# Kernel tuning notes

Measured on AMD Instinct MI355X. Metric: run time of the kernel, lower is better.

The kernel has to match this reference:

```python
import jax, jax.numpy as jnp
import numpy as np

B, S, D = 2, 2048, 2048
H = 16
KV_RANK = 512
NOPE, ROPE = 128, 64
QK_HD = NOPE + ROPE  # 192
V_HD = 128
SCALE = QK_HD ** -0.5
EPS = 1.1920929e-07  # torch RMSNorm default eps = finfo(fp32).eps
NEG = -1e9


def rmsnorm(x, w):
    return x * jax.lax.rsqrt(jnp.mean(x * x, axis=-1, keepdims=True) + EPS) * w


def apply_rope(x, freqs):
    # x: (b, s, h, r) interleaved pairs; freqs: (s, r//2) angles
    sh = x.shape
    xr = x.reshape(*sh[:-1], -1, 2)
    a, b = xr[..., 0], xr[..., 1]
    cos = jnp.cos(freqs)[None, :, None, :]
    sin = jnp.sin(freqs)[None, :, None, :]
    return jnp.stack([a * cos - b * sin, a * sin + b * cos], axis=-1).reshape(sh)


def setup_inputs() -> dict:
    key = jax.random.key(0)
    ks = jax.random.split(key, 8)
    inv = lambda k, shape, fan_in: jax.random.uniform(k, shape, jnp.float32, -1.0, 1.0) / np.sqrt(fan_in)
    x = jax.random.normal(ks[0], (B, S, D), jnp.float32)
    freqs = jax.random.uniform(ks[1], (S, ROPE // 2), jnp.float32) * np.float32(np.pi)
    mask = jnp.where(jnp.triu(jnp.ones((S, S), bool), k=1), jnp.float32(NEG), jnp.float32(0.0))
    wq_w = inv(ks[2], (H * QK_HD, D), D)
    wq_b = jnp.zeros((H * QK_HD,), jnp.float32)
    wkv_a_w = inv(ks[3], (KV_RANK + ROPE, D), D)
    wkv_a_b = jnp.zeros((KV_RANK + ROPE,), jnp.float32)
    kv_norm_w = jnp.ones((KV_RANK,), jnp.float32)
    wkv_b_w = inv(ks[4], (H * (NOPE + V_HD), KV_RANK), KV_RANK)
    wo_w = inv(ks[5], (D, H * V_HD), H * V_HD)
    wo_b = jnp.zeros((D,), jnp.float32)
    return dict(x=x, freqs=freqs, mask=mask, wq_w=wq_w, wq_b=wq_b,
                wkv_a_w=wkv_a_w, wkv_a_b=wkv_a_b, kv_norm_w=kv_norm_w,
                wkv_b_w=wkv_b_w, wo_w=wo_w, wo_b=wo_b)


def reference(x, freqs, mask, wq_w, wq_b, wkv_a_w, wkv_a_b, kv_norm_w, wkv_b_w, wo_w, wo_b):
    b, s, _ = x.shape
    # q projection (q_lora_rank == 0 path)
    q = (x @ wq_w.T + wq_b).reshape(b, s, H, QK_HD)
    q_nope, q_pe = q[..., :NOPE], q[..., NOPE:]
    q_pe = apply_rope(q_pe, freqs)
    # latent kv projection
    kv = x @ wkv_a_w.T + wkv_a_b
    kv, k_pe = kv[..., :KV_RANK], kv[..., KV_RANK:]
    k_pe = apply_rope(k_pe[:, :, None, :], freqs)[:, :, 0, :]  # (b, t, r)
    kv_proj = rmsnorm(kv, kv_norm_w)  # (b, t, c)
    wkv_b = wkv_b_w.reshape(H, NOPE + V_HD, KV_RANK)
    # absorb K-nope projection into q
    q_nope = jnp.einsum('bshd,hdc->bshc', q_nope, wkv_b[:, :NOPE])
    scores = (jnp.einsum('bshc,btc->bsht', q_nope, kv_proj)
              + jnp.einsum('bshr,btr->bsht', q_pe, k_pe)) * SCALE
    scores = scores + mask[None, :, None, :]
    scores = jax.nn.softmax(scores.astype(jnp.float32), axis=-1).astype(x.dtype)
    out = jnp.einsum('bsht,btc->bshc', scores, kv_proj)
    out = jnp.einsum('bshc,hdc->bshd', out, wkv_b[:, -V_HD:])
    return out.reshape(b, s, H * V_HD) @ wo_w.T + wo_b
```

## Files before the change

kernel.cpp:

```cpp
#include <hip/hip_runtime.h>
#include <hip/hip_bf16.h>
#include <math.h>

#define B_ 2
#define S_ 2048
#define H_ 16
#define SCALE_ 0.07216878364870323f
#define SL2_ (0.07216878364870323f * 1.4426950408889634f)
#define EPS_ 1.1920929e-07f
#define M0_ 8.0f

typedef __attribute__((ext_vector_type(8))) short bf16x8;
typedef __attribute__((ext_vector_type(4))) float f32x4;
union U4 { uint4 u; bf16x8 v; f32x4 f; };

__device__ __forceinline__ uint bfbits(float x) {
    uint u = __float_as_uint(x);
    return (u + 0x7fffu + ((u >> 16) & 1u)) >> 16;
}
__device__ __forceinline__ uint pack2bf(float a, float b) {
    return bfbits(a) | (bfbits(b) << 16);
}
__device__ __forceinline__ uint cvtpk(float a, float b) {
    uint r;
    asm("v_cvt_pk_bf16_f32 %0, %1, %2" : "=v"(r) : "v"(a), "v"(b));
    return r;
}
__device__ __forceinline__ void gld_lds16(const ushort* g, ushort* l) {
    __builtin_amdgcn_global_load_lds(
        (const __attribute__((address_space(1))) uint*)g,
        (__attribute__((address_space(3))) uint*)l, 16, 0, 0);
}

template<bool OUT_BF16>
__global__ __launch_bounds__(256) void mgemm(
    const ushort* __restrict__ A, int lda, long long aOff1, long long aOff2,
    const ushort* __restrict__ Bm, int ldb, long long bOff1, long long bOff2,
    const float* __restrict__ bias, float scale,
    void* __restrict__ Cv, int ldc, long long cOff1, long long cOff2,
    int K, int zDiv)
{
    __shared__ ushort As[128 * 32];
    __shared__ ushort Bs[128 * 32];

    const int z = blockIdx.z;
    const int z1 = z % zDiv, z2 = z / zDiv;
    A  += z1 * aOff1 + z2 * aOff2;
    Bm += z1 * bOff1 + z2 * bOff2;
    const long long cBase = z1 * cOff1 + z2 * cOff2;

    const int n0 = blockIdx.x * 128;
    const int m0 = blockIdx.y * 128;
    const int tid = threadIdx.x;
    const int w   = tid >> 6;
    const int l   = tid & 63;
    const int m   = l & 15;
    const int q4  = l >> 4;
    const int mw  = (w & 1) * 64;
    const int nw  = (w >> 1) * 64;
    const int sr  = l >> 2;
    const int sc  = l & 3;

    f32x4 acc[4][4];
#pragma unroll
    for (int i = 0; i < 4; ++i)
#pragma unroll
        for (int j = 0; j < 4; ++j) acc[i][j] = (f32x4){0.f, 0.f, 0.f, 0.f};

    for (int k0 = 0; k0 < K; k0 += 32) {
#pragma unroll
        for (int jj = 0; jj < 2; ++jj) {
            const int slot = w * 2 + jj;
            const int row  = slot * 16 + sr;
            const int g    = sc ^ ((row >> 1) & 3);
            gld_lds16(&A[(long long)(m0 + row) * lda + k0 + g * 8], &As[slot * 512]);
            gld_lds16(&Bm[(long long)(n0 + row) * ldb + k0 + g * 8], &Bs[slot * 512]);
        }
        __syncthreads();

        U4 af[4], bf[4];
#pragma unroll
        for (int i = 0; i < 4; ++i) {
            const int ra = mw + i * 16 + m;
            af[i].u = *(const uint4*)&As[ra * 32 + (q4 ^ ((ra >> 1) & 3)) * 8];
            const int rb = nw + i * 16 + m;
            bf[i].u = *(const uint4*)&Bs[rb * 32 + (q4 ^ ((rb >> 1) & 3)) * 8];
        }
#pragma unroll
        for (int i = 0; i < 4; ++i)
#pragma unroll
            for (int j = 0; j < 4; ++j)
                acc[i][j] = __builtin_amdgcn_mfma_f32_16x16x32_bf16(
                    af[i].v, bf[j].v, acc[i][j], 0, 0, 0);
        __syncthreads();
    }

#pragma unroll
    for (int j = 0; j < 4; ++j) {
        const int cn = n0 + nw + j * 16 + m;
        const float bv = bias ? bias[cn] : 0.0f;
#pragma unroll
        for (int i = 0; i < 4; ++i) {
            const int rw = m0 + mw + i * 16 + q4 * 4;
#pragma unroll
            for (int r = 0; r < 4; ++r) {
                const float val = acc[i][j][r] * scale + bv;
                if (OUT_BF16)
                    ((ushort*)Cv)[cBase + (long long)(rw + r) * ldc + cn] =
                        (ushort)bfbits(val);
                else
                    ((float*)Cv)[cBase + (long long)(rw + r) * ldc + cn] = val;
            }
        }
    }
}

__global__ __launch_bounds__(256) void conv_all(
    const float* __restrict__ x, const float* __restrict__ wq,
    const float* __restrict__ wkva, const float* __restrict__ wo,
    const float* __restrict__ wkvb,
    ushort* __restrict__ x_bf, ushort* __restrict__ wq_bf,
    ushort* __restrict__ wkva_bf, ushort* __restrict__ wo_bf,
    ushort* __restrict__ wkvbK, ushort* __restrict__ wkvbV)
{
    const int bid = blockIdx.x;
    const int tid = threadIdx.x;
    if (bid < 8192) {
        const long long i = ((long long)bid * 256 + tid) * 4;
        float4 v = *(const float4*)&x[i];
        uint2 p; p.x = pack2bf(v.x, v.y); p.y = pack2bf(v.z, v.w);
        *(uint2*)&x_bf[i] = p;
    } else if (bid < 14336) {
        const long long i = ((long long)(bid - 8192) * 256 + tid) * 4;
        float4 v = *(const float4*)&wq[i];
        uint2 p; p.x = pack2bf(v.x, v.y); p.y = pack2bf(v.z, v.w);
        *(uint2*)&wq_bf[i] = p;
    } else if (bid < 15616) {
        const int i = ((bid - 14336) * 256 + tid) * 4;
        const int r = i >> 11;
        uint2 p = make_uint2(0u, 0u);
        if (r < 576) {
            float4 v = *(const float4*)&wkva[i];
            p.x = pack2bf(v.x, v.y); p.y = pack2bf(v.z, v.w);
        }
        *(uint2*)&wkva_bf[i] = p;
    } else if (bid < 19712) {
        const long long i = ((long long)(bid - 15616) * 256 + tid) * 4;
        float4 v = *(const float4*)&wo[i];
        uint2 p; p.x = pack2bf(v.x, v.y); p.y = pack2bf(v.z, v.w);
        *(uint2*)&wo_bf[i] = p;
    } else if (bid < 20736) {
        const int i = ((bid - 19712) * 256 + tid) * 4;
        const int h = i >> 16, rem = i & 65535;
        float4 v = *(const float4*)&wkvb[((long long)(h * 256)) * 512 + rem];
        uint2 p; p.x = pack2bf(v.x, v.y); p.y = pack2bf(v.z, v.w);
        *(uint2*)&wkvbK[i] = p;
    } else {
        const int i = ((bid - 20736) * 256 + tid) * 4;
        const int h = i >> 16, rem = i & 65535;
        float4 v = *(const float4*)&wkvb[((long long)(h * 256 + 128)) * 512 + rem];
        uint2 p; p.x = pack2bf(v.x, v.y); p.y = pack2bf(v.z, v.w);
        *(uint2*)&wkvbV[i] = p;
    }
}

__global__ __launch_bounds__(256) void qprep(
    const float* __restrict__ q_raw, const float* __restrict__ freqs,
    ushort* __restrict__ q192)
{
    const int idx = blockIdx.x * 256 + threadIdx.x;
    const int row = idx / 48;
    const int c4  = idx % 48;
    const int bs = row >> 4, h = row & 15;
    const float* src = q_raw + (long long)bs * 3072 + h * 192;
    if (c4 < 32) {
        const int d = c4 * 4;
        float4 v = *(const float4*)&src[d];
        uint2 p;
        p.x = pack2bf(v.x * SL2_, v.y * SL2_);
        p.y = pack2bf(v.z * SL2_, v.w * SL2_);
        *(uint2*)&q192[(long long)row * 192 + d] = p;
    } else {
        const int j = c4 - 32;
        const int s = bs & 2047;
        const float f0 = freqs[s * 32 + j * 2];
        const float f1 = freqs[s * 32 + j * 2 + 1];
        float c0, s0, c1, s1;
        __sincosf(f0, &s0, &c0);
        __sincosf(f1, &s1, &c1);
        float4 v = *(const float4*)&src[128 + j * 4];
        uint2 p;
        p.x = pack2bf((v.x * c0 - v.y * s0) * SL2_, (v.x * s0 + v.y * c0) * SL2_);
        p.y = pack2bf((v.z * c1 - v.w * s1) * SL2_, (v.z * s1 + v.w * c1) * SL2_);
        *(uint2*)&q192[(long long)row * 192 + 128 + j * 4] = p;
    }
}

__global__ __launch_bounds__(64) void kv_post_kernel(
    const float* __restrict__ kv_raw, const float* __restrict__ bias,
    const float* __restrict__ w, const float* __restrict__ freqs,
    ushort* __restrict__ kv_h)
{
    const int bs = blockIdx.x;
    const int lane = threadIdx.x;
    const float* src = kv_raw + (long long)bs * 640;
    ushort* dst = kv_h + (long long)bs * 576;

    const int c = 4 * lane;
    float4 v0 = *(const float4*)&src[c];
    float4 v1 = *(const float4*)&src[256 + c];
    float4 b0 = *(const float4*)&bias[c];
    float4 b1 = *(const float4*)&bias[256 + c];
    v0.x += b0.x; v0.y += b0.y; v0.z += b0.z; v0.w += b0.w;
    v1.x += b1.x; v1.y += b1.y; v1.z += b1.z; v1.w += b1.w;
    float ss = v0.x * v0.x + v0.y * v0.y + v0.z * v0.z + v0.w * v0.w +
               v1.x * v1.x + v1.y * v1.y + v1.z * v1.z + v1.w * v1.w;
#pragma unroll
    for (int o = 32; o; o >>= 1) ss += __shfl_xor(ss, o, 64);
    const float rs = rsqrtf(ss * (1.0f / 512.0f) + EPS_);

    float4 w0 = *(const float4*)&w[c];
    float4 w1 = *(const float4*)&w[256 + c];
    uint2 p0, p1;
    p0.x = pack2bf(v0.x * rs * w0.x, v0.y * rs * w0.y);
    p0.y = pack2bf(v0.z * rs * w0.z, v0.w * rs * w0.w);
    p1.x = pack2bf(v1.x * rs * w1.x, v1.y * rs * w1.y);
    p1.y = pack2bf(v1.z * rs * w1.z, v1.w * rs * w1.w);
    *(uint2*)&dst[c] = p0;
    *(uint2*)&dst[256 + c] = p1;

    if (lane < 32) {
        const int s = bs & 2047;
        const float f = freqs[s * 32 + lane];
        float cs, sn;
        __sincosf(f, &sn, &cs);
        const float a  = src[512 + 2 * lane]     + bias[512 + 2 * lane];
        const float b2 = src[512 + 2 * lane + 1] + bias[512 + 2 * lane + 1];
        *(uint*)&dst[512 + 2 * lane] = pack2bf(a * cs - b2 * sn, a * sn + b2 * cs);
    }
}

__global__ __launch_bounds__(256) void prep_all(
    const ushort* __restrict__ K_h, const ushort* __restrict__ V_hT,
    const ushort* __restrict__ kv_h,
    uint4* __restrict__ khimg, uint4* __restrict__ vhimg,
    uint4* __restrict__ rimg)
{
    const int bid = blockIdx.x;
    if (bid < 4096) {
        const int g = bid * 256 + threadIdx.x;
        const int lane = g & 63, ck = (g >> 6) & 7, h = (g >> 9) & 15;
        const int tile = (g >> 13) & 63, b = g >> 19;
        const int m = lane & 15, q4 = lane >> 4, f = ck >> 1, s = ck & 1;
        const uint4 v = *(const uint4*)&K_h[
            ((long long)(b * S_ + tile * 32 + s * 16 + m)) * 2048 + h * 128 + f * 32 + q4 * 8];
        khimg[(((long long)(b * 64 + tile) * 16 + h) * 8 + ck) * 64 + lane] = v;
    } else if (bid < 8192) {
        const int g = (bid - 4096) * 256 + threadIdx.x;
        const int lane = g & 63, c = (g >> 6) & 7, h = (g >> 9) & 15;
        const int tile = (g >> 13) & 63, b = g >> 19;
        const int m = lane & 15, q4 = lane >> 4;
        const uint4 v = *(const uint4*)&V_hT[
            ((long long)((b * 16 + h) * 128 + c * 16 + m)) * 2048 + tile * 32 + q4 * 8];
        vhimg[(((long long)(b * 64 + tile) * 16 + h) * 8 + c) * 64 + lane] = v;
    } else {
        const int g = (bid - 8192) * 256 + threadIdx.x;
        const int lane = g & 63, ck = (g >> 6) & 3, tile = (g >> 8) & 63, b = g >> 14;
        const int m = lane & 15, q4 = lane >> 4, f2 = ck >> 1, s = ck & 1;
        const uint4 v = *(const uint4*)&kv_h[
            ((long long)(b * S_ + tile * 32 + s * 16 + m)) * 576 + 512 + f2 * 32 + q4 * 8];
        rimg[((long long)(b * 64 + tile) * 4 + ck) * 64 + lane] = v;
    }
}

__global__ __launch_bounds__(256, 2) void attn_kernel(
    const ushort* __restrict__ q192,
    const uint4*  __restrict__ khimg,
    const uint4*  __restrict__ rimg,
    const uint4*  __restrict__ vhimg,
    ushort* __restrict__ o_h)
{
    __shared__ uint buf[2][20 * 256];

    const int p    = blockIdx.x;
    const int h    = blockIdx.y;
    const int b    = blockIdx.z;
    const int tid  = threadIdx.x;
    const int wid  = tid >> 6;
    const int lane = tid & 63;
    const int m    = lane & 15;
    const int q4   = lane >> 4;
    const bool odd = q4 & 1;

    auto stage = [&](int bs, int it) {
        const long long tb = (long long)(b * 64 + it);
        const uint4* kb = khimg + ((tb * 16 + h) * 8) * 64;
        const uint4* rb = rimg  + (tb * 4) * 64;
        const uint4* vb = vhimg + ((tb * 16 + h) * 8) * 64;
        ushort* l = (ushort*)&buf[bs][0];
        gld_lds16((const ushort*)(kb + (wid    ) * 64 + lane), l + (wid     ) * 512);
        gld_lds16((const ushort*)(kb + (wid + 4) * 64 + lane), l + (wid +  4) * 512);
        gld_lds16((const ushort*)(rb + (wid    ) * 64 + lane), l + (wid +  8) * 512);
        gld_lds16((const ushort*)(vb + (wid    ) * 64 + lane), l + (wid + 12) * 512);
        gld_lds16((const ushort*)(vb + (wid + 4) * 64 + lane), l + (wid + 16) * 512);
    };

    int cur = 0;
    for (int pass = 0; pass < 2; ++pass) {
        const int chunk = pass ? p : (15 - p);
        const int row0a = chunk * 128 + wid * 16;
        const int row0b = row0a + 64;
        const int sRa   = row0a + m;
        const int sRb   = row0b + m;

        U4 qfa[6], qfb[6];
        {
            const uint4* qpa = (const uint4*)(q192 + ((long long)(b * S_ + sRa) * H_ + h) * 192);
            const uint4* qpb = (const uint4*)(q192 + ((long long)(b * S_ + sRb) * H_ + h) * 192);
#pragma unroll
            for (int f = 0; f < 6; ++f) { qfa[f].u = qpa[f * 4 + q4]; qfb[f].u = qpb[f * 4 + q4]; }
        }

        f32x4 oA[8], oB[8];
#pragma unroll
        for (int c = 0; c < 8; ++c) {
            oA[c] = (f32x4){0.f, 0.f, 0.f, 0.f};
            oB[c] = (f32x4){0.f, 0.f, 0.f, 0.f};
        }
        float lA = 0.0f, lB = 0.0f;

        auto softpack = [&](const f32x4 s0, const f32x4 s1, int t0v, int rw0,
                            float& lac) -> U4 {
            float p00, p01, p02, p03, p10, p11, p12, p13;
            if (t0v + 31 <= rw0) {
                p00 = exp2f(s0[0] - M0_); p01 = exp2f(s0[1] - M0_);
                p02 = exp2f(s0[2] - M0_); p03 = exp2f(s0[3] - M0_);
                p10 = exp2f(s1[0] - M0_); p11 = exp2f(s1[1] - M0_);
                p12 = exp2f(s1[2] - M0_); p13 = exp2f(s1[3] - M0_);
            } else {
                const int sR = rw0 + m;
                const int tb0 = t0v + q4 * 4;
                const int tb1 = tb0 + 16;
                p00 = (tb0 + 0 <= sR) ? exp2f(s0[0] - M0_) : 0.0f;
                p01 = (tb0 + 1 <= sR) ? exp2f(s0[1] - M0_) : 0.0f;
                p02 = (tb0 + 2 <= sR) ? exp2f(s0[2] - M0_) : 0.0f;
                p03 = (tb0 + 3 <= sR) ? exp2f(s0[3] - M0_) : 0.0f;
                p10 = (tb1 + 0 <= sR) ? exp2f(s1[0] - M0_) : 0.0f;
                p11 = (tb1 + 1 <= sR) ? exp2f(s1[1] - M0_) : 0.0f;
                p12 = (tb1 + 2 <= sR) ? exp2f(s1[2] - M0_) : 0.0f;
                p13 = (tb1 + 3 <= sR) ? exp2f(s1[3] - M0_) : 0.0f;
            }
            lac += (p00 + p01) + (p02 + p03) + (p10 + p11) + (p12 + p13);
            uint X0 = cvtpk(p00, p01), X1 = cvtpk(p02, p03);
            uint Y0 = cvtpk(p10, p11), Y1 = cvtpk(p12, p13);
            asm("v_permlane32_swap_b32 %0, %1" : "+v"(X0), "+v"(Y0));
            asm("v_permlane32_swap_b32 %0, %1" : "+v"(X1), "+v"(Y1));
            uint u0 = odd ? X0 : Y0;
            uint u1 = odd ? X1 : Y1;
            uint w0 = (uint)__builtin_amdgcn_ds_swizzle((int)u0, 0x401F);
            uint w1 = (uint)__builtin_amdgcn_ds_swizzle((int)u1, 0x401F);
            U4 bb;
            bb.u.x = odd ? w0 : X0;
            bb.u.y = odd ? w1 : X1;
            bb.u.z = odd ? Y0 : w0;
            bb.u.w = odd ? Y1 : w1;
            return bb;
        };

        const int nT = chunk * 4 + 4;
        __syncthreads();
        stage(cur, 0);

        for (int it = 0; it < nT; ++it) {
            const int t0 = it * 32;
            __syncthreads();
            if (it + 1 < nT) stage(cur ^ 1, it + 1);
            __builtin_amdgcn_sched_barrier(0);

            const uint* bb0 = &buf[cur][0];
            const int abase = lane * 4;
            const bool liveB = (t0 <= row0b + 15);
            const bool liveA = (t0 <= row0a + 15);
            const bool twoA  = (t0 < row0a);
            const bool twoB  = (t0 < row0b);

            if (liveB) {
                f32x4 sA0 = (f32x4){0.f,0.f,0.f,0.f}, sA1 = (f32x4){0.f,0.f,0.f,0.f};
                f32x4 sB0 = (f32x4){0.f,0.f,0.f,0.f}, sB1 = (f32x4){0.f,0.f,0.f,0.f};

                if (twoA) {
#pragma unroll
                    for (int f = 0; f < 6; ++f) {
                        const int ck = (f < 4) ? f * 2 : (f - 4) * 2 + 8;
                        U4 a0, a1;
                        a0.u = *(const uint4*)&bb0[ck * 256 + abase];
                        a1.u = *(const uint4*)&bb0[(ck + 1) * 256 + abase];
                        sA0 = __builtin_amdgcn_mfma_f32_16x16x32_bf16(a0.v, qfa[f].v, sA0, 0, 0, 0);
                        sB0 = __builtin_amdgcn_mfma_f32_16x16x32_bf16(a0.v, qfb[f].v, sB0, 0, 0, 0);
                        sA1 = __builtin_amdgcn_mfma_f32_16x16x32_bf16(a1.v, qfa[f].v, sA1, 0, 0, 0);
                        sB1 = __builtin_amdgcn_mfma_f32_16x16x32_bf16(a1.v, qfb[f].v, sB1, 0, 0, 0);
                    }
                } else {
#pragma unroll
                    for (int f = 0; f < 6; ++f) {
                        const int ck = (f < 4) ? f * 2 : (f - 4) * 2 + 8;
                        U4 a0;
                        a0.u = *(const uint4*)&bb0[ck * 256 + abase];
                        if (liveA)
                            sA0 = __builtin_amdgcn_mfma_f32_16x16x32_bf16(a0.v, qfa[f].v, sA0, 0, 0, 0);
                        sB0 = __builtin_amdgcn_mfma_f32_16x16x32_bf16(a0.v, qfb[f].v, sB0, 0, 0, 0);
                        if (twoB) {
                            U4 a1;
                            a1.u = *(const uint4*)&bb0[(ck + 1) * 256 + abase];
                            sB1 = __builtin_amdgcn_mfma_f32_16x16x32_bf16(a1.v, qfb[f].v, sB1, 0, 0, 0);
                        }
                    }
                }

                U4 bbB = softpack(sB0, sB1, t0, row0b, lB);
                if (liveA) {
                    U4 bbA = softpack(sA0, sA1, t0, row0a, lA);
#pragma unroll
                    for (int c = 0; c < 8; ++c) {
                        U4 av; av.u = *(const uint4*)&bb0[(12 + c) * 256 + abase];
                        oB[c] = __builtin_amdgcn_mfma_f32_16x16x32_bf16(av.v, bbB.v, oB[c], 0, 0, 0);
                        oA[c] = __builtin_amdgcn_mfma_f32_16x16x32_bf16(av.v, bbA.v, oA[c], 0, 0, 0);
                    }
                } else {
#pragma unroll
                    for (int c = 0; c < 8; ++c) {
                        U4 av; av.u = *(const uint4*)&bb0[(12 + c) * 256 + abase];
                        oB[c] = __builtin_amdgcn_mfma_f32_16x16x32_bf16(av.v, bbB.v, oB[c], 0, 0, 0);
                    }
                }
            }
            cur ^= 1;
        }

        lA += __shfl_xor(lA, 16, 64);
        lA += __shfl_xor(lA, 32, 64);
        lB += __shfl_xor(lB, 16, 64);
        lB += __shfl_xor(lB, 32, 64);
        const float invA = 1.0f / lA;
        const float invB = 1.0f / lB;

        ushort* opa = o_h + ((long long)(b * S_ + sRa) * H_ + h) * 128;
        ushort* opb = o_h + ((long long)(b * S_ + sRb) * H_ + h) * 128;
#pragma unroll
        for (int c = 0; c < 8; ++c) {
            uint2 pva, pvb;
            pva.x = cvtpk(oA[c][0] * invA, oA[c][1] * invA);
            pva.y = cvtpk(oA[c][2] * invA, oA[c][3] * invA);
            pvb.x = cvtpk(oB[c][0] * invB, oB[c][1] * invB);
            pvb.y = cvtpk(oB[c][2] * invB, oB[c][3] * invB);
            *(uint2*)&opa[c * 16 + q4 * 4] = pva;
            *(uint2*)&opb[c * 16 + q4 * 4] = pvb;
        }
    }
}

extern "C" void kernel_launch(void* const* d_in, const int* in_sizes, int n_in,
                              void* d_out, int out_size, void* d_ws, size_t ws_size,
                              hipStream_t stream)
{
    const float* x         = (const float*)d_in[0];
    const float* freqs     = (const float*)d_in[1];
    const float* wq_w      = (const float*)d_in[3];
    const float* wq_b      = (const float*)d_in[4];
    const float* wkv_a_w   = (const float*)d_in[5];
    const float* wkv_a_b   = (const float*)d_in[6];
    const float* kv_norm_w = (const float*)d_in[7];
    const float* wkv_b_w   = (const float*)d_in[8];
    const float* wo_w      = (const float*)d_in[9];
    const float* wo_b      = (const float*)d_in[10];
    float* out = (float*)d_out;

    char* w = (char*)d_ws;
    ushort* x_bf    = (ushort*)w;  w += 16777216;
    ushort* wq_bf   = (ushort*)w;  w += 12582912;
    ushort* wkva_bf = (ushort*)w;  w += 2621440;
    ushort* wo_bf   = (ushort*)w;  w += 8388608;
    ushort* wkvbK   = (ushort*)w;  w += 2097152;
    ushort* wkvbV   = (ushort*)w;  w += 2097152;
    float*  kv_raw  = (float*)w;   w += 10485760;
    ushort* kv_h    = (ushort*)w;  w += 4718592;
    ushort* K_h     = (ushort*)w;  w += 16777216;
    ushort* V_hT    = (ushort*)w;  w += 16777216;
    uint4*  khimg   = (uint4*)w;   w += 16777216;
    uint4*  vhimg   = (uint4*)w;   w += 16777216;
    uint4*  rimg    = (uint4*)w;   w += 524288;
    char* RA = w;                  w += 50331648;
    float*  q_raw = (float*)RA;
    ushort* o_h   = (ushort*)RA;
    ushort* q192  = (ushort*)w;    w += 25165824;

    dim3 blk(256);

    conv_all<<<dim3(21760), blk, 0, stream>>>(
        x, wq_w, wkv_a_w, wo_w, wkv_b_w,
        x_bf, wq_bf, wkva_bf, wo_bf, wkvbK, wkvbV);

    mgemm<false><<<dim3(24, 32, 1), blk, 0, stream>>>(
        x_bf, 2048, 0LL, 0LL, wq_bf, 2048, 0LL, 0LL, wq_b, 1.0f,
        q_raw, 3072, 0LL, 0LL, 2048, 1);

    mgemm<false><<<dim3(5, 32, 1), blk, 0, stream>>>(
        x_bf, 2048, 0LL, 0LL, wkva_bf, 2048, 0LL, 0LL, nullptr, 1.0f,
        kv_raw, 640, 0LL, 0LL, 2048, 1);

    qprep<<<dim3(12288), blk, 0, stream>>>(q_raw, freqs, q192);

    kv_post_kernel<<<dim3(4096), dim3(64), 0, stream>>>(
        kv_raw, wkv_a_b, kv_norm_w, freqs, kv_h);

    mgemm<true><<<dim3(1, 16, 32), blk, 0, stream>>>(
        kv_h, 576, 0LL, (long long)S_ * 576,
        wkvbK, 512, 65536LL, 0LL, nullptr, 1.0f,
        K_h, 2048, 128LL, (long long)S_ * 2048, 512, 16);
    mgemm<true><<<dim3(16, 1, 32), blk, 0, stream>>>(
        wkvbV, 512, 65536LL, 0LL,
        kv_h, 576, 0LL, (long long)S_ * 576, nullptr, 1.0f,
        V_hT, 2048, 262144LL, 4194304LL, 512, 16);

    prep_all<<<dim3(8320), blk, 0, stream>>>(K_h, V_hT, kv_h, khimg, vhimg, rimg);

    attn_kernel<<<dim3(8, 16, 2), blk, 0, stream>>>(q192, khimg, rimg, vhimg, o_h);

    mgemm<false><<<dim3(16, 32, 1), blk, 0, stream>>>(
        o_h, 2048, 0LL, 0LL, wo_bf, 2048, 0LL, 0LL, wo_b, 1.0f,
        out, 2048, 0LL, 0LL, 2048, 1);
}
```

Measured before the change: 483.7 us.

## Split attention KV loop across two blocks and combine partial outputs

Doubles the attention grid by having each block process only even or odd KV tiles, writing unnormalized fp32 partial outputs and row sums to scratch. A new combine kernel sums the two partials, normalizes and writes bf16 output. It relies on the fixed max (M0_) softmax, so partials add directly without rescaling. It adds extra fp32 traffic and a launch, and the workspace layout is reshuffled so scratch buffers alias.

After: 466.0 us. 3.7% less time.

```diff
diff --git a/kernel.cpp b/kernel.cpp
--- a/kernel.cpp
+++ b/kernel.cpp
@@ -278,13 +278,16 @@
     const uint4*  __restrict__ khimg,
     const uint4*  __restrict__ rimg,
     const uint4*  __restrict__ vhimg,
-    ushort* __restrict__ o_h)
+    float* __restrict__ part_o,
+    float* __restrict__ part_l)
 {
     __shared__ uint buf[2][20 * 256];
 
     const int p    = blockIdx.x;
     const int h    = blockIdx.y;
-    const int b    = blockIdx.z;
+    const int zz   = blockIdx.z;
+    const int b    = zz >> 1;
+    const int par  = zz & 1;
     const int tid  = threadIdx.x;
     const int wid  = tid >> 6;
     const int lane = tid & 63;
@@ -367,14 +370,15 @@
             return bb;
         };
 
-        const int nT = chunk * 4 + 4;
+        const int nT2 = 2 * chunk + 2;
         __syncthreads();
-        stage(cur, 0);
-
-        for (int it = 0; it < nT; ++it) {
+        stage(cur, par);
+
+        for (int v = 0; v < nT2; ++v) {
+            const int it = 2 * v + par;
             const int t0 = it * 32;
             __syncthreads();
-            if (it + 1 < nT) stage(cur ^ 1, it + 1);
+            if (v + 1 < nT2) stage(cur ^ 1, it + 2);
             __builtin_amdgcn_sched_barrier(0);
 
             const uint* bb0 = &buf[cur][0];
@@ -441,22 +445,43 @@
         lA += __shfl_xor(lA, 32, 64);
         lB += __shfl_xor(lB, 16, 64);
         lB += __shfl_xor(lB, 32, 64);
-        const float invA = 1.0f / lA;
-        const float invB = 1.0f / lB;
-
-        ushort* opa = o_h + ((long long)(b * S_ + sRa) * H_ + h) * 128;
-        ushort* opb = o_h + ((long long)(b * S_ + sRb) * H_ + h) * 128;
+
+        const int cid  = (b * 16 + h) * 16 + chunk;
+        const int slot = cid * 2 + par;
+        float* po = part_o + (long long)slot * 16384;
+        const int rA = wid * 16 + m;
+        const int rB = rA + 64;
 #pragma unroll
         for (int c = 0; c < 8; ++c) {
-            uint2 pva, pvb;
-            pva.x = cvtpk(oA[c][0] * invA, oA[c][1] * invA);
-            pva.y = cvtpk(oA[c][2] * invA, oA[c][3] * invA);
-            pvb.x = cvtpk(oB[c][0] * invB, oB[c][1] * invB);
-            pvb.y = cvtpk(oB[c][2] * invB, oB[c][3] * invB);
-            *(uint2*)&opa[c * 16 + q4 * 4] = pva;
-            *(uint2*)&opb[c * 16 + q4 * 4] = pvb;
-        }
-    }
+            *(f32x4*)&po[rA * 128 + c * 16 + q4 * 4] = oA[c];
+            *(f32x4*)&po[rB * 128 + c * 16 + q4 * 4] = oB[c];
+        }
+        if (q4 == 0) {
+            part_l[slot * 128 + rA] = lA;
+            part_l[slot * 128 + rB] = lB;
+        }
+    }
+}
+
+__global__ __launch_bounds__(256) void combine_kernel(
+    const float* __restrict__ part_o, const float* __restrict__ part_l,
+    ushort* __restrict__ o_h)
+{
+    const int idx = blockIdx.x * 256 + threadIdx.x;
+    const int d4  = (idx & 31) * 4;
+    const int r   = (idx >> 5) & 127;
+    const int cid = idx >> 12;
+    const int chunk = cid & 15, h = (cid >> 4) & 15, b = cid >> 8;
+    const long long s0 = (long long)(cid * 2) * 16384 + r * 128 + d4;
+    float4 a = *(const float4*)&part_o[s0];
+    float4 c = *(const float4*)&part_o[s0 + 16384];
+    const float l = part_l[cid * 256 + r] + part_l[cid * 256 + 128 + r];
+    const float inv = 1.0f / l;
+    uint2 pk;
+    pk.x = cvtpk((a.x + c.x) * inv, (a.y + c.y) * inv);
+    pk.y = cvtpk((a.z + c.z) * inv, (a.w + c.w) * inv);
+    const int s = chunk * 128 + r;
+    *(uint2*)&o_h[(((long long)(b * S_ + s)) * H_ + h) * 128 + d4] = pk;
 }
 
 extern "C" void kernel_launch(void* const* d_in, const int* in_sizes, int n_in,
@@ -476,23 +501,25 @@
     float* out = (float*)d_out;
 
     char* w = (char*)d_ws;
-    ushort* x_bf    = (ushort*)w;  w += 16777216;
-    ushort* wq_bf   = (ushort*)w;  w += 12582912;
-    ushort* wkva_bf = (ushort*)w;  w += 2621440;
     ushort* wo_bf   = (ushort*)w;  w += 8388608;
-    ushort* wkvbK   = (ushort*)w;  w += 2097152;
-    ushort* wkvbV   = (ushort*)w;  w += 2097152;
-    float*  kv_raw  = (float*)w;   w += 10485760;
-    ushort* kv_h    = (ushort*)w;  w += 4718592;
-    ushort* K_h     = (ushort*)w;  w += 16777216;
-    ushort* V_hT    = (ushort*)w;  w += 16777216;
     uint4*  khimg   = (uint4*)w;   w += 16777216;
     uint4*  vhimg   = (uint4*)w;   w += 16777216;
     uint4*  rimg    = (uint4*)w;   w += 524288;
-    char* RA = w;                  w += 50331648;
-    float*  q_raw = (float*)RA;
-    ushort* o_h   = (ushort*)RA;
-    ushort* q192  = (ushort*)w;    w += 25165824;
+    ushort* q192    = (ushort*)w;  w += 25165824;
+    ushort* o_h     = (ushort*)w;  w += 16777216;
+    char* SCR = w;
+    ushort* x_bf    = (ushort*)(SCR);
+    ushort* wq_bf   = (ushort*)(SCR + 16777216);
+    ushort* wkva_bf = (ushort*)(SCR + 29360128);
+    ushort* wkvbK   = (ushort*)(SCR + 31981568);
+    ushort* wkvbV   = (ushort*)(SCR + 34078720);
+    float*  kv_raw  = (float*)(SCR + 36175872);
+    float*  q_raw   = (float*)(SCR + 46661632);
+    ushort* kv_h    = (ushort*)(SCR);
+    ushort* K_h     = (ushort*)(SCR + 4718592);
+    ushort* V_hT    = (ushort*)(SCR + 36175872);
+    float*  part_o  = (float*)(SCR);
+    float*  part_l  = (float*)(SCR + 67108864);
 
     dim3 blk(256);
 
@@ -524,7 +551,10 @@
 
     prep_all<<<dim3(8320), blk, 0, stream>>>(K_h, V_hT, kv_h, khimg, vhimg, rimg);
 
-    attn_kernel<<<dim3(8, 16, 2), blk, 0, stream>>>(q192, khimg, rimg, vhimg, o_h);
+    attn_kernel<<<dim3(8, 16, 4), blk, 0, stream>>>(
+        q192, khimg, rimg, vhimg, part_o, part_l);
+
+    combine_kernel<<<dim3(8192), blk, 0, stream>>>(part_o, part_l, o_h);
 
     mgemm<false><<<dim3(16, 32, 1), blk, 0, stream>>>(
         o_h, 2048, 0LL, 0LL, wo_bf, 2048, 0LL, 0LL, wo_b, 1.0f,
```
